# Kernel optimization log

Measured on AMD Instinct MI355X. Metric: run time of the kernel, lower is better.

The kernel has to match this reference:

```python
import jax, jax.numpy as jnp
import numpy as np
from jax import lax

DROP_PROB = 0.1
BLOCK_SIZE = 7
FEAT_SIZE = 56
GAMMA = DROP_PROB / BLOCK_SIZE ** 2 * (FEAT_SIZE ** 2 / (FEAT_SIZE - BLOCK_SIZE + 1) ** 2)


def setup_inputs() -> dict:
    key = jax.random.key(0)
    k1, k2 = jax.random.split(key)
    x = jax.random.normal(k1, (32, 256, 56, 56), dtype=jnp.float32)
    u = jax.random.uniform(k2, (56, 56), dtype=jnp.float32)
    return {"x": x, "u": u}


def reference(x, u):
    # Bernoulli(gamma) seed mask over (H, W)
    mask = (u < GAMMA).astype(x.dtype)
    # Original code scatters 1s at seed + offsets in [0, block)^2 (down/right),
    # then crops to (H, W). Equivalent: backward-looking max window of size block.
    dilated = lax.reduce_window(
        mask, jnp.array(0.0, x.dtype), lax.max,
        window_dimensions=(BLOCK_SIZE, BLOCK_SIZE),
        window_strides=(1, 1),
        padding=((BLOCK_SIZE - 1, 0), (BLOCK_SIZE - 1, 0)),
    )
    block_mask = 1.0 - dilated  # (H, W), 0 inside dropped blocks
    scale = block_mask.size / jnp.sum(block_mask)
    return x * block_mask[None, None, :, :] * scale
```

## Files before the change

kernel.cpp:

```cpp
#include <hip/hip_runtime.h>


#define HW      3136
#define WDIM    56
#define HDIM    56
#define HW4     784
#define ROWMASK 0x00FFFFFFFFFFFFFFull
#define NBLOCKS 2009u
#define STRIDE  (NBLOCKS * 256u)

typedef float vfloat4 __attribute__((ext_vector_type(4)));

__global__ void __launch_bounds__(256) dropblock_fused_kernel(
        const float* __restrict__ u, const vfloat4* __restrict__ x,
        vfloat4* __restrict__ out, unsigned int nvec) {
    __shared__ unsigned long long chunks[49];
    __shared__ unsigned long long dropbits[HDIM];
    __shared__ float s_scale;

    const float gamma = (float)(0.1 / 49.0 * (3136.0 / 2500.0));

    const unsigned int t = blockIdx.x * 256u + threadIdx.x;

    vfloat4 a0 = x[t];
    vfloat4 a1 = x[t + STRIDE];

    const int lane = threadIdx.x & 63;
    const int wave = threadIdx.x >> 6;

    #pragma unroll
    for (int k = 0; k < 12; ++k) {
        unsigned long long b = __ballot(u[k * 256 + threadIdx.x] < gamma);
        if (lane == 0) chunks[4 * k + wave] = b;
    }
    if (wave == 0) {
        unsigned long long b = __ballot(u[3072 + lane] < gamma);
        if (lane == 0) chunks[48] = b;
    }
    __syncthreads();

    if (wave == 0) {
        const int r = lane;
        unsigned long long rd = 0ull;
        if (r < HDIM) {
            int bit = r * WDIM;
            int a = bit >> 6, off = bit & 63;
            unsigned long long row = chunks[a] >> off;
            if (off > 8) row |= chunks[a + 1] << (64 - off);
            row &= ROWMASK;
            rd = row;
            #pragma unroll
            for (int k = 1; k < 7; ++k) rd |= row << k;
            rd &= ROWMASK;
        }
        unsigned long long d = rd;
        #pragma unroll
        for (int k = 1; k <= 6; ++k)
            d |= __shfl_up(rd, k);
        int kept = 0;
        if (r < HDIM) {
            dropbits[r] = d;
            kept = WDIM - __popcll(d);
        }
        #pragma unroll
        for (int s = 32; s; s >>= 1) kept += __shfl_xor(kept, s);
        if (lane == 0) s_scale = (float)HW / (float)kept;
    }
    __syncthreads();

    {
        const unsigned int q = t % (unsigned int)HW4;
        const int r = (int)q / 14;
        const int c0 = ((int)q - r * 14) * 4;
        const unsigned long long d = dropbits[r];
        const float scale = s_scale;
        vfloat4 m;
        m[0] = ((d >> c0) & 1ull) ? 0.0f : scale;
        m[1] = ((d >> (c0 + 1)) & 1ull) ? 0.0f : scale;
        m[2] = ((d >> (c0 + 2)) & 1ull) ? 0.0f : scale;
        m[3] = ((d >> (c0 + 3)) & 1ull) ? 0.0f : scale;

        out[t] = a0 * m;
        out[t + STRIDE] = a1 * m;
        unsigned int i = t + 2u * STRIDE;
        for (; i + STRIDE < nvec; i += 2u * STRIDE) {
            vfloat4 b0 = x[i];
            vfloat4 b1 = x[i + STRIDE];
            out[i] = b0 * m;
            out[i + STRIDE] = b1 * m;
        }
        if (i < nvec) out[i] = x[i] * m;
    }
}

extern "C" void kernel_launch(void* const* d_in, const int* in_sizes, int n_in,
                              void* d_out, int out_size, void* d_ws, size_t ws_size,
                              hipStream_t stream) {
    const float* x = (const float*)d_in[0];
    const float* u = (const float*)d_in[1];
    float* out = (float*)d_out;

    unsigned int nvec = (unsigned int)(out_size / 4);
    dropblock_fused_kernel<<<NBLOCKS, 256, 0, stream>>>(
        u, (const vfloat4*)x, (vfloat4*)out, nvec);
}
```

Before: 185.8 us.

## Fully unroll streaming loop with hardcoded sizes, early u loads, nontemporal stores

Hardcodes the total vector count and stride so each thread handles a fixed 12-13 vectors in a fully unrolled sequence. Loads of x are issued in batches of four ahead of the stores, and all u loads are hoisted before the ballots. Stores become nontemporal, and launch bounds request 8 blocks per CU. This aims to raise memory-level parallelism and cut cache pollution from the output, but the kernel now only works for this one input shape and uses more registers.

```diff
diff --git a/kernel.cpp b/kernel.cpp
--- a/kernel.cpp
+++ b/kernel.cpp
@@ -7,13 +7,15 @@
 #define HW4     784
 #define ROWMASK 0x00FFFFFFFFFFFFFFull
 #define NBLOCKS 2009u
-#define STRIDE  (NBLOCKS * 256u)
+#define STRIDE  514304u
+#define NVEC    6422528u
+#define REM     250880u
 
 typedef float vfloat4 __attribute__((ext_vector_type(4)));
 
-__global__ void __launch_bounds__(256) dropblock_fused_kernel(
+__global__ void __launch_bounds__(256, 8) dropblock_fused_kernel(
         const float* __restrict__ u, const vfloat4* __restrict__ x,
-        vfloat4* __restrict__ out, unsigned int nvec) {
+        vfloat4* __restrict__ out) {
     __shared__ unsigned long long chunks[49];
     __shared__ unsigned long long dropbits[HDIM];
     __shared__ float s_scale;
@@ -21,21 +23,47 @@
     const float gamma = (float)(0.1 / 49.0 * (3136.0 / 2500.0));
 
     const unsigned int t = blockIdx.x * 256u + threadIdx.x;
+    const int lane = threadIdx.x & 63;
+    const int wave = threadIdx.x >> 6;
+
+    float u0  = u[threadIdx.x];
+    float u1  = u[threadIdx.x + 256];
+    float u2  = u[threadIdx.x + 512];
+    float u3  = u[threadIdx.x + 768];
+    float u4  = u[threadIdx.x + 1024];
+    float u5  = u[threadIdx.x + 1280];
+    float u6  = u[threadIdx.x + 1536];
+    float u7  = u[threadIdx.x + 1792];
+    float u8  = u[threadIdx.x + 2048];
+    float u9  = u[threadIdx.x + 2304];
+    float u10 = u[threadIdx.x + 2560];
+    float u11 = u[threadIdx.x + 2816];
+    float ulast = 0.0f;
+    if (wave == 0) ulast = u[3072 + lane];
 
     vfloat4 a0 = x[t];
     vfloat4 a1 = x[t + STRIDE];
+    vfloat4 a2 = x[t + 2u * STRIDE];
+    vfloat4 a3 = x[t + 3u * STRIDE];
 
-    const int lane = threadIdx.x & 63;
-    const int wave = threadIdx.x >> 6;
-
-    #pragma unroll
-    for (int k = 0; k < 12; ++k) {
-        unsigned long long b = __ballot(u[k * 256 + threadIdx.x] < gamma);
-        if (lane == 0) chunks[4 * k + wave] = b;
-    }
-    if (wave == 0) {
-        unsigned long long b = __ballot(u[3072 + lane] < gamma);
-        if (lane == 0) chunks[48] = b;
+    {
+        unsigned long long b;
+        b = __ballot(u0  < gamma); if (lane == 0) chunks[ 0 + wave] = b;
+        b = __ballot(u1  < gamma); if (lane == 0) chunks[ 4 + wave] = b;
+        b = __ballot(u2  < gamma); if (lane == 0) chunks[ 8 + wave] = b;
+        b = __ballot(u3  < gamma); if (lane == 0) chunks[12 + wave] = b;
+        b = __ballot(u4  < gamma); if (lane == 0) chunks[16 + wave] = b;
+        b = __ballot(u5  < gamma); if (lane == 0) chunks[20 + wave] = b;
+        b = __ballot(u6  < gamma); if (lane == 0) chunks[24 + wave] = b;
+        b = __ballot(u7  < gamma); if (lane == 0) chunks[28 + wave] = b;
+        b = __ballot(u8  < gamma); if (lane == 0) chunks[32 + wave] = b;
+        b = __ballot(u9  < gamma); if (lane == 0) chunks[36 + wave] = b;
+        b = __ballot(u10 < gamma); if (lane == 0) chunks[40 + wave] = b;
+        b = __ballot(u11 < gamma); if (lane == 0) chunks[44 + wave] = b;
+        if (wave == 0) {
+            b = __ballot(ulast < gamma);
+            if (lane == 0) chunks[48] = b;
+        }
     }
     __syncthreads();
 
@@ -68,29 +96,44 @@
     }
     __syncthreads();
 
+    vfloat4 m;
     {
         const unsigned int q = t % (unsigned int)HW4;
         const int r = (int)q / 14;
         const int c0 = ((int)q - r * 14) * 4;
         const unsigned long long d = dropbits[r];
         const float scale = s_scale;
-        vfloat4 m;
         m[0] = ((d >> c0) & 1ull) ? 0.0f : scale;
         m[1] = ((d >> (c0 + 1)) & 1ull) ? 0.0f : scale;
         m[2] = ((d >> (c0 + 2)) & 1ull) ? 0.0f : scale;
         m[3] = ((d >> (c0 + 3)) & 1ull) ? 0.0f : scale;
+    }
 
-        out[t] = a0 * m;
-        out[t + STRIDE] = a1 * m;
-        unsigned int i = t + 2u * STRIDE;
-        for (; i + STRIDE < nvec; i += 2u * STRIDE) {
-            vfloat4 b0 = x[i];
-            vfloat4 b1 = x[i + STRIDE];
-            out[i] = b0 * m;
-            out[i + STRIDE] = b1 * m;
-        }
-        if (i < nvec) out[i] = x[i] * m;
-    }
+    const bool ht = t < REM;
+
+    vfloat4 b0 = x[t + 4u * STRIDE];
+    vfloat4 b1 = x[t + 5u * STRIDE];
+    vfloat4 b2 = x[t + 6u * STRIDE];
+    vfloat4 b3 = x[t + 7u * STRIDE];
+    __builtin_nontemporal_store(a0 * m, &out[t]);
+    __builtin_nontemporal_store(a1 * m, &out[t + STRIDE]);
+    __builtin_nontemporal_store(a2 * m, &out[t + 2u * STRIDE]);
+    __builtin_nontemporal_store(a3 * m, &out[t + 3u * STRIDE]);
+    vfloat4 c0 = x[t + 8u * STRIDE];
+    vfloat4 c1 = x[t + 9u * STRIDE];
+    vfloat4 c2 = x[t + 10u * STRIDE];
+    vfloat4 c3 = x[t + 11u * STRIDE];
+    vfloat4 d0;
+    if (ht) d0 = x[t + 12u * STRIDE];
+    __builtin_nontemporal_store(b0 * m, &out[t + 4u * STRIDE]);
+    __builtin_nontemporal_store(b1 * m, &out[t + 5u * STRIDE]);
+    __builtin_nontemporal_store(b2 * m, &out[t + 6u * STRIDE]);
+    __builtin_nontemporal_store(b3 * m, &out[t + 7u * STRIDE]);
+    __builtin_nontemporal_store(c0 * m, &out[t + 8u * STRIDE]);
+    __builtin_nontemporal_store(c1 * m, &out[t + 9u * STRIDE]);
+    __builtin_nontemporal_store(c2 * m, &out[t + 10u * STRIDE]);
+    __builtin_nontemporal_store(c3 * m, &out[t + 11u * STRIDE]);
+    if (ht) __builtin_nontemporal_store(d0 * m, &out[t + 12u * STRIDE]);
 }
 
 extern "C" void kernel_launch(void* const* d_in, const int* in_sizes, int n_in,
@@ -100,7 +143,6 @@
     const float* u = (const float*)d_in[1];
     float* out = (float*)d_out;
 
-    unsigned int nvec = (unsigned int)(out_size / 4);
     dropblock_fused_kernel<<<NBLOCKS, 256, 0, stream>>>(
-        u, (const vfloat4*)x, (vfloat4*)out, nvec);
+        u, (const vfloat4*)x, (vfloat4*)out);
 }
```

Result: no change. 184.8 us (-0.5%).

## Split mask build into a single-block kernel and stream x with nontemporal stores

Applied to the files above, without the earlier changes.

The dropblock mask is now computed once by a single-block kernel and written to workspace. A separate streaming kernel then multiplies x by that precomputed mask, with each thread handling four float4 elements and using nontemporal stores. This removes the mask reconstruction that every block repeated in the fused kernel and shortens the loop to a fixed unroll. The cost is a second kernel launch with a serial dependency, and the element count is hardcoded, so other shapes are not handled.

```diff
diff --git a/kernel.cpp b/kernel.cpp
--- a/kernel.cpp
+++ b/kernel.cpp
@@ -6,24 +6,19 @@
 #define HDIM    56
 #define HW4     784
 #define ROWMASK 0x00FFFFFFFFFFFFFFull
-#define NBLOCKS 2009u
-#define STRIDE  (NBLOCKS * 256u)
+#define NB      6272u
+#define NT      1605632u
+#define NVEC    6422528u
 
 typedef float vfloat4 __attribute__((ext_vector_type(4)));
 
-__global__ void __launch_bounds__(256) dropblock_fused_kernel(
-        const float* __restrict__ u, const vfloat4* __restrict__ x,
-        vfloat4* __restrict__ out, unsigned int nvec) {
+__global__ void __launch_bounds__(256) dropblock_mask_kernel(
+        const float* __restrict__ u, vfloat4* __restrict__ m4) {
     __shared__ unsigned long long chunks[49];
     __shared__ unsigned long long dropbits[HDIM];
     __shared__ float s_scale;
 
     const float gamma = (float)(0.1 / 49.0 * (3136.0 / 2500.0));
-
-    const unsigned int t = blockIdx.x * 256u + threadIdx.x;
-
-    vfloat4 a0 = x[t];
-    vfloat4 a1 = x[t + STRIDE];
 
     const int lane = threadIdx.x & 63;
     const int wave = threadIdx.x >> 6;
@@ -69,28 +64,34 @@
     __syncthreads();
 
     {
-        const unsigned int q = t % (unsigned int)HW4;
-        const int r = (int)q / 14;
-        const int c0 = ((int)q - r * 14) * 4;
-        const unsigned long long d = dropbits[r];
         const float scale = s_scale;
-        vfloat4 m;
-        m[0] = ((d >> c0) & 1ull) ? 0.0f : scale;
-        m[1] = ((d >> (c0 + 1)) & 1ull) ? 0.0f : scale;
-        m[2] = ((d >> (c0 + 2)) & 1ull) ? 0.0f : scale;
-        m[3] = ((d >> (c0 + 3)) & 1ull) ? 0.0f : scale;
+        for (int q = threadIdx.x; q < HW4; q += 256) {
+            const int r = q / 14;
+            const int c0 = (q - r * 14) * 4;
+            const unsigned long long d = dropbits[r];
+            vfloat4 m;
+            m[0] = ((d >> c0) & 1ull) ? 0.0f : scale;
+            m[1] = ((d >> (c0 + 1)) & 1ull) ? 0.0f : scale;
+            m[2] = ((d >> (c0 + 2)) & 1ull) ? 0.0f : scale;
+            m[3] = ((d >> (c0 + 3)) & 1ull) ? 0.0f : scale;
+            m4[q] = m;
+        }
+    }
+}
 
-        out[t] = a0 * m;
-        out[t + STRIDE] = a1 * m;
-        unsigned int i = t + 2u * STRIDE;
-        for (; i + STRIDE < nvec; i += 2u * STRIDE) {
-            vfloat4 b0 = x[i];
-            vfloat4 b1 = x[i + STRIDE];
-            out[i] = b0 * m;
-            out[i + STRIDE] = b1 * m;
-        }
-        if (i < nvec) out[i] = x[i] * m;
-    }
+__global__ void __launch_bounds__(256) dropblock_stream_kernel(
+        const vfloat4* __restrict__ x, vfloat4* __restrict__ out,
+        const vfloat4* __restrict__ m4) {
+    const unsigned int t = blockIdx.x * 256u + threadIdx.x;
+    const vfloat4 m = m4[t % (unsigned int)HW4];
+    const vfloat4 a0 = x[t];
+    const vfloat4 a1 = x[t + NT];
+    const vfloat4 a2 = x[t + 2u * NT];
+    const vfloat4 a3 = x[t + 3u * NT];
+    __builtin_nontemporal_store(a0 * m, &out[t]);
+    __builtin_nontemporal_store(a1 * m, &out[t + NT]);
+    __builtin_nontemporal_store(a2 * m, &out[t + 2u * NT]);
+    __builtin_nontemporal_store(a3 * m, &out[t + 3u * NT]);
 }
 
 extern "C" void kernel_launch(void* const* d_in, const int* in_sizes, int n_in,
@@ -99,8 +100,9 @@
     const float* x = (const float*)d_in[0];
     const float* u = (const float*)d_in[1];
     float* out = (float*)d_out;
+    vfloat4* m4 = (vfloat4*)d_ws;
 
-    unsigned int nvec = (unsigned int)(out_size / 4);
-    dropblock_fused_kernel<<<NBLOCKS, 256, 0, stream>>>(
-        u, (const vfloat4*)x, (vfloat4*)out, nvec);
+    dropblock_mask_kernel<<<1, 256, 0, stream>>>(u, m4);
+    dropblock_stream_kernel<<<NB, 256, 0, stream>>>(
+        (const vfloat4*)x, (vfloat4*)out, m4);
 }
```

Result: slower. 192.5 us (+3.6%).
